# Performance work log

Hardware: AMD Instinct MI355X
Metric: run time of the kernel (lower is better)

The kernel has to match this reference:

```python
import jax, jax.numpy as jnp
import numpy as np

B, C, D, H, CS = 2, 1024, 512, 8, 64  # batch, bindings, d_binding, heads, chunk_size


def setup_inputs() -> dict:
    key = jax.random.key(0)
    ks = jax.random.split(key, 12)
    d = D // H
    def lin(k, out_f, in_f):
        return jax.random.normal(k, (out_f, in_f), jnp.float32) * (1.0 / np.sqrt(in_f))
    return {
        "x": jax.random.normal(ks[0], (B, C, D), jnp.float32),
        "Wq": lin(ks[1], D, D), "bq": jnp.zeros((D,), jnp.float32),
        "Wk": lin(ks[2], D, D), "bk": jnp.zeros((D,), jnp.float32),
        "Wv": lin(ks[3], D, D), "bv": jnp.zeros((D,), jnp.float32),
        "w1": lin(ks[4], d, 3 * d), "b1": jnp.zeros((d,), jnp.float32),
        "w2": lin(ks[5], 1, d), "b2": jnp.zeros((1,), jnp.float32),
        "Wo": lin(ks[6], D, D), "bo": jnp.zeros((D,), jnp.float32),
    }


def reference(x, Wq, bq, Wk, bk, Wv, bv, w1, b1, w2, b2, Wo, bo):
    Bx, Cx, Dx = x.shape
    d = Dx // H
    def heads(W, b):
        y = jnp.einsum('bcD,eD->bce', x, W) + b
        return y.reshape(Bx, Cx, H, d).transpose(0, 2, 1, 3)  # (B,H,C,d)
    q = heads(Wq, bq)
    k = heads(Wk, bk)
    v = heads(Wv, bv)
    # split first MLP layer weight into q / k / q*k blocks
    w1_q, w1_k, w1_qk = w1[:, :d], w1[:, d:2 * d], w1[:, 2 * d:]
    qp = jnp.einsum('bhcd,ed->bhce', q, w1_q)  # (B,H,C,d)
    kp = jnp.einsum('bhcd,ed->bhce', k, w1_k)  # (B,H,C,d)
    nc = Cx // CS
    q_ch = q.reshape(Bx, H, nc, CS, d).transpose(2, 0, 1, 3, 4)   # (nc,B,H,CS,d)
    qp_ch = qp.reshape(Bx, H, nc, CS, d).transpose(2, 0, 1, 3, 4)
    inv_sqrt_d = jnp.float32(1.0 / np.sqrt(d))

    def step(carry, xs):
        qc, qpc = xs  # (B,H,CS,d) each
        # hidden: (B,H,CS,C,d)
        res = qpc[:, :, :, None, :] + kp[:, :, None, :, :] + b1
        inter = qc[:, :, :, None, :] * k[:, :, None, :, :]
        hid = res + jnp.einsum('bhijd,ed->bhije', inter, w1_qk)
        h = jax.nn.gelu(hid, approximate=False)
        scores = (jnp.einsum('bhije,e->bhij', h, w2[0]) + b2[0]) * inv_sqrt_d
        attn = jax.nn.softmax(scores, axis=-1)  # (B,H,CS,C)
        out = jnp.einsum('bhij,bhjd->bhid', attn, v)  # (B,H,CS,d)
        return carry, out

    _, outs = jax.lax.scan(jax.checkpoint(step), None, (q_ch, qp_ch))  # (nc,B,H,CS,d)
    out = outs.transpose(1, 2, 0, 3, 4).reshape(Bx, H, Cx, d)
    out = out.transpose(0, 2, 1, 3).reshape(Bx, Cx, Dx)
    return jnp.einsum('bcD,eD->bce', out, Wo) + bo
```

## Files before the change

### kernel.cpp

```cpp
#include <hip/hip_runtime.h>
#include <cstdint>

typedef unsigned short u16;
typedef unsigned int u32;
typedef __attribute__((ext_vector_type(8))) short short8;
typedef __attribute__((ext_vector_type(4))) float floatx4;

__device__ __forceinline__ float b2f(u16 u) {
    union { unsigned int i; float f; } c; c.i = ((unsigned int)u) << 16; return c.f;
}
__device__ __forceinline__ u16 f2b(float f) {
    union { float f; unsigned int i; } c; c.f = f;
    unsigned int u = c.i;
    u = u + 0x7FFFu + ((u >> 16) & 1u);
    return (u16)(u >> 16);
}
__device__ __forceinline__ float rdlane(float v, int l) {
    union { float f; int i; } c; c.f = v;
    union { int i; float f; } o; o.i = __builtin_amdgcn_readlane(c.i, l);
    return o.f;
}
__device__ __forceinline__ float u2f(u32 u) { union { u32 u; float f; } c; c.u = u; return c.f; }

__global__ __launch_bounds__(256) void gemm_qkv(
    const float* __restrict__ x,
    const float* __restrict__ Wq, const float* __restrict__ Wk, const float* __restrict__ Wv,
    const float* __restrict__ bq, const float* __restrict__ bk, const float* __restrict__ bv,
    float* __restrict__ qout, u16* __restrict__ kout, float* __restrict__ vout)
{
    __shared__ u16 xs[64 * 72];
    __shared__ u16 wsl[64 * 72];
    int tid = threadIdx.x;
    int lane = tid & 63;
    int wv = tid >> 6;
    int lo = lane & 15, hi = lane >> 4;
    int which = blockIdx.y >> 3;
    int m0 = blockIdx.x * 64, n0 = (blockIdx.y & 7) * 64;
    const float* W    = which == 0 ? Wq : (which == 1 ? Wk : Wv);
    const float* bias = which == 0 ? bq : (which == 1 ? bk : bv);

    floatx4 acc[4];
#pragma unroll
    for (int mt = 0; mt < 4; ++mt) acc[mt] = (floatx4){0.f, 0.f, 0.f, 0.f};

    for (int k0 = 0; k0 < 512; k0 += 64) {
        __syncthreads();
#pragma unroll
        for (int i = 0; i < 2; ++i) {
            int v = tid + i * 256;
            int row = v >> 3, c8 = (v & 7) * 8;
            const float* ap = x + (m0 + row) * 512 + k0 + c8;
            const float* wp = W + (n0 + row) * 512 + k0 + c8;
            float4 a0 = *(const float4*)(ap);
            float4 a1 = *(const float4*)(ap + 4);
            float4 w0 = *(const float4*)(wp);
            float4 w1v = *(const float4*)(wp + 4);
            union { u16 u[8]; uint4 q; } ca, cw;
            ca.u[0] = f2b(a0.x); ca.u[1] = f2b(a0.y); ca.u[2] = f2b(a0.z); ca.u[3] = f2b(a0.w);
            ca.u[4] = f2b(a1.x); ca.u[5] = f2b(a1.y); ca.u[6] = f2b(a1.z); ca.u[7] = f2b(a1.w);
            cw.u[0] = f2b(w0.x); cw.u[1] = f2b(w0.y); cw.u[2] = f2b(w0.z); cw.u[3] = f2b(w0.w);
            cw.u[4] = f2b(w1v.x); cw.u[5] = f2b(w1v.y); cw.u[6] = f2b(w1v.z); cw.u[7] = f2b(w1v.w);
            *(uint4*)(xs + row * 72 + c8)  = ca.q;
            *(uint4*)(wsl + row * 72 + c8) = cw.q;
        }
        __syncthreads();
#pragma unroll
        for (int ks = 0; ks < 2; ++ks) {
            short8 bfr = *(const short8*)(wsl + (wv * 16 + lo) * 72 + ks * 32 + hi * 8);
#pragma unroll
            for (int mt = 0; mt < 4; ++mt) {
                short8 afr = *(const short8*)(xs + (mt * 16 + lo) * 72 + ks * 32 + hi * 8);
                acc[mt] = __builtin_amdgcn_mfma_f32_16x16x32_bf16(afr, bfr, acc[mt], 0, 0, 0);
            }
        }
    }

    int n = n0 + wv * 16 + lo;
    float bv2 = bias[n];
    int h = n >> 6, dd = n & 63;
#pragma unroll
    for (int mt = 0; mt < 4; ++mt) {
#pragma unroll
        for (int r = 0; r < 4; ++r) {
            int m = m0 + mt * 16 + hi * 4 + r;
            float y = acc[mt][r] + bv2;
            int b = m >> 10, c = m & 1023;
            int idx = (((b * 8 + h) * 1024) + c) * 64 + dd;
            if (which == 0)      qout[idx] = y;
            else if (which == 1) kout[idx] = f2b(y);
            else                 vout[idx] = y;
        }
    }
}

__global__ __launch_bounds__(256) void gemm_out(
    const float* __restrict__ A, const float* __restrict__ W, const float* __restrict__ bias,
    float* __restrict__ outf)
{
    __shared__ u16 xs[64 * 72];
    __shared__ u16 wsl[64 * 72];
    int tid = threadIdx.x;
    int lane = tid & 63;
    int wv = tid >> 6;
    int lo = lane & 15, hi = lane >> 4;
    int m0 = blockIdx.x * 64, n0 = blockIdx.y * 64;

    floatx4 acc[4];
#pragma unroll
    for (int mt = 0; mt < 4; ++mt) acc[mt] = (floatx4){0.f, 0.f, 0.f, 0.f};

    for (int k0 = 0; k0 < 512; k0 += 64) {
        __syncthreads();
#pragma unroll
        for (int i = 0; i < 2; ++i) {
            int v = tid + i * 256;
            int row = v >> 3, c8 = (v & 7) * 8;
            const float* ap = A + (m0 + row) * 512 + k0 + c8;
            const float* wp = W + (n0 + row) * 512 + k0 + c8;
            float4 a0 = *(const float4*)(ap);
            float4 a1 = *(const float4*)(ap + 4);
            float4 w0 = *(const float4*)(wp);
            float4 w1v = *(const float4*)(wp + 4);
            union { u16 u[8]; uint4 q; } ca, cw;
            ca.u[0] = f2b(a0.x); ca.u[1] = f2b(a0.y); ca.u[2] = f2b(a0.z); ca.u[3] = f2b(a0.w);
            ca.u[4] = f2b(a1.x); ca.u[5] = f2b(a1.y); ca.u[6] = f2b(a1.z); ca.u[7] = f2b(a1.w);
            cw.u[0] = f2b(w0.x); cw.u[1] = f2b(w0.y); cw.u[2] = f2b(w0.z); cw.u[3] = f2b(w0.w);
            cw.u[4] = f2b(w1v.x); cw.u[5] = f2b(w1v.y); cw.u[6] = f2b(w1v.z); cw.u[7] = f2b(w1v.w);
            *(uint4*)(xs + row * 72 + c8)  = ca.q;
            *(uint4*)(wsl + row * 72 + c8) = cw.q;
        }
        __syncthreads();
#pragma unroll
        for (int ks = 0; ks < 2; ++ks) {
            short8 bfr = *(const short8*)(wsl + (wv * 16 + lo) * 72 + ks * 32 + hi * 8);
#pragma unroll
            for (int mt = 0; mt < 4; ++mt) {
                short8 afr = *(const short8*)(xs + (mt * 16 + lo) * 72 + ks * 32 + hi * 8);
                acc[mt] = __builtin_amdgcn_mfma_f32_16x16x32_bf16(afr, bfr, acc[mt], 0, 0, 0);
            }
        }
    }

    int n = n0 + wv * 16 + lo;
    float bv = bias[n];
#pragma unroll
    for (int mt = 0; mt < 4; ++mt)
#pragma unroll
        for (int r = 0; r < 4; ++r) {
            int m = m0 + mt * 16 + hi * 4 + r;
            outf[m * 512 + n] = acc[mt][r] + bv;
        }
}

__global__ __launch_bounds__(256, 4) void attn13(
    const float* __restrict__ qf, const u16* __restrict__ kb, const float* __restrict__ vf,
    const float* __restrict__ w1, const float* __restrict__ b1, const float* __restrict__ w2,
    float* __restrict__ ao)
{
    __shared__ float q_l[4 * 64];
    int tid = threadIdx.x;
    int lane = tid & 63;
    int wv = tid >> 6;
    int lo = lane & 15, hi = lane >> 4;
    int bh = blockIdx.x >> 8;
    int qi = ((blockIdx.x & 255) << 2) | wv;

    const float NA = -2.45546696f;

    q_l[wv * 64 + lane] = qf[(bh * 1024 + qi) * 64 + lane];

    float qpacc = b1[lane];
#pragma unroll
    for (int d8 = 0; d8 < 64; d8 += 8) {
        float4 wa = *(const float4*)(w1 + lane * 192 + d8);
        float4 wb = *(const float4*)(w1 + lane * 192 + d8 + 4);
        const float* q8 = q_l + wv * 64 + d8;
        qpacc = __builtin_fmaf(q8[0], wa.x, qpacc);
        qpacc = __builtin_fmaf(q8[1], wa.y, qpacc);
        qpacc = __builtin_fmaf(q8[2], wa.z, qpacc);
        qpacc = __builtin_fmaf(q8[3], wa.w, qpacc);
        qpacc = __builtin_fmaf(q8[4], wb.x, qpacc);
        qpacc = __builtin_fmaf(q8[5], wb.y, qpacc);
        qpacc = __builtin_fmaf(q8[6], wb.z, qpacc);
        qpacc = __builtin_fmaf(q8[7], wb.w, qpacc);
    }
    qpacc *= NA;

    u32 wcp[4][2];
    float w2row = w2[lane] * -0.07344288f;
#pragma unroll
    for (int mt = 0; mt < 4; ++mt)
#pragma unroll
        for (int h2 = 0; h2 < 2; ++h2) {
            int e0 = mt * 16 + hi * 4 + h2 * 2;
            u32 lo16 = (u32)f2b(__shfl(w2row, e0));
            u32 hi16 = (u32)f2b(__shfl(w2row, e0 + 1));
            wcp[mt][h2] = (hi16 << 16) | lo16;
        }

    float qv2[2][8];
#pragma unroll
    for (int ks = 0; ks < 2; ++ks)
#pragma unroll
        for (int j = 0; j < 8; ++j)
            qv2[ks][j] = q_l[wv * 64 + ks * 32 + hi * 8 + j];

    short8 af[4][2];
#pragma unroll
    for (int mt = 0; mt < 4; ++mt) {
        const float* wr = w1 + (mt * 16 + lo) * 192;
#pragma unroll
        for (int ks = 0; ks < 2; ++ks) {
            int dd0 = ks * 32 + hi * 8;
            float4 a0 = *(const float4*)(wr + 128 + dd0);
            float4 a1 = *(const float4*)(wr + 128 + dd0 + 4);
            float4 k0 = *(const float4*)(wr + 64 + dd0);
            float4 k1 = *(const float4*)(wr + 64 + dd0 + 4);
            union { u16 u[8]; short8 s; } cv;
            cv.u[0] = f2b(NA * __builtin_fmaf(qv2[ks][0], a0.x, k0.x));
            cv.u[1] = f2b(NA * __builtin_fmaf(qv2[ks][1], a0.y, k0.y));
            cv.u[2] = f2b(NA * __builtin_fmaf(qv2[ks][2], a0.z, k0.z));
            cv.u[3] = f2b(NA * __builtin_fmaf(qv2[ks][3], a0.w, k0.w));
            cv.u[4] = f2b(NA * __builtin_fmaf(qv2[ks][4], a1.x, k1.x));
            cv.u[5] = f2b(NA * __builtin_fmaf(qv2[ks][5], a1.y, k1.y));
            cv.u[6] = f2b(NA * __builtin_fmaf(qv2[ks][6], a1.z, k1.z));
            cv.u[7] = f2b(NA * __builtin_fmaf(qv2[ks][7], a1.w, k1.w));
            af[mt][ks] = cv.s;
        }
    }

    floatx4 qpinit[4];
    {
        const floatx4 z = (floatx4){0.f, 0.f, 0.f, 0.f};
        union { u16 u[8]; short8 s; } bb;
#pragma unroll
        for (int i = 0; i < 8; ++i) bb.u[i] = 0;
        bb.u[0] = (hi == 0) ? (u16)0x3F80 : (u16)0;
#pragma unroll
        for (int mt = 0; mt < 4; ++mt) {
            float qpv = __shfl(qpacc, mt * 16 + lo);
            union { u16 u[8]; short8 s; } aa;
#pragma unroll
            for (int i = 0; i < 8; ++i) aa.u[i] = 0;
            aa.u[0] = (hi == 0) ? f2b(qpv) : (u16)0;
            qpinit[mt] = __builtin_amdgcn_mfma_f32_16x16x32_bf16(aa.s, bb.s, z, 0, 0, 0);
        }
    }

    float l_run = 0.f;
    float oa0 = 0.f, oa1 = 0.f, oa2 = 0.f, oa3 = 0.f;
    const u16*   kbase = kb + bh * 65536;
    const float* vbase = vf + bh * 65536;

    short8 bf[2][2];
#pragma unroll
    for (int t = 0; t < 2; ++t)
#pragma unroll
        for (int ks = 0; ks < 2; ++ks) {
            uint4 kv = *(const uint4*)(kbase + (t * 16 + lo) * 64 + ks * 32 + hi * 8);
            bf[t][ks] = *(short8*)&kv;
        }

    for (int j0 = 0; j0 < 1024; j0 += 32) {
        float s0a = 0.f, s0b = 0.f, s1a = 0.f, s1b = 0.f;

        floatx4 aP[2], aN[2];
        aP[0] = __builtin_amdgcn_mfma_f32_16x16x32_bf16(af[0][0], bf[0][0], qpinit[0], 0, 0, 0);
        aP[0] = __builtin_amdgcn_mfma_f32_16x16x32_bf16(af[0][1], bf[0][1], aP[0], 0, 0, 0);
        aP[1] = __builtin_amdgcn_mfma_f32_16x16x32_bf16(af[0][0], bf[1][0], qpinit[0], 0, 0, 0);
        aP[1] = __builtin_amdgcn_mfma_f32_16x16x32_bf16(af[0][1], bf[1][1], aP[1], 0, 0, 0);

#pragma unroll
        for (int mt = 0; mt < 4; ++mt) {
            if (mt < 3) {
                aN[0] = __builtin_amdgcn_mfma_f32_16x16x32_bf16(af[mt + 1][0], bf[0][0], qpinit[mt + 1], 0, 0, 0);
                aN[0] = __builtin_amdgcn_mfma_f32_16x16x32_bf16(af[mt + 1][1], bf[0][1], aN[0], 0, 0, 0);
                aN[1] = __builtin_amdgcn_mfma_f32_16x16x32_bf16(af[mt + 1][0], bf[1][0], qpinit[mt + 1], 0, 0, 0);
                aN[1] = __builtin_amdgcn_mfma_f32_16x16x32_bf16(af[mt + 1][1], bf[1][1], aN[1], 0, 0, 0);
            } else {
                int jn = (j0 + 32) & 1023;
#pragma unroll
                for (int t = 0; t < 2; ++t)
#pragma unroll
                    for (int ks = 0; ks < 2; ++ks) {
                        uint4 kv = *(const uint4*)(kbase + (jn + t * 16 + lo) * 64 + ks * 32 + hi * 8);
                        bf[t][ks] = *(short8*)&kv;
                    }
            }

#pragma unroll
            for (int h2 = 0; h2 < 2; ++h2) {
                u32 wp = wcp[mt][h2];
                float w0 = u2f(wp << 16);
                float w1v = u2f(wp & 0xFFFF0000u);
#pragma unroll
                for (int t = 0; t < 2; ++t) {
                    float x0 = aP[t][h2 * 2 + 0];
                    float x1 = aP[t][h2 * 2 + 1];
                    float a0 = 1.0f + __builtin_amdgcn_exp2f(x0);
                    float a1 = 1.0f + __builtin_amdgcn_exp2f(x1);
                    float rc = __builtin_amdgcn_rcpf(a0 * a1);
                    if (t == 0) {
                        s0a = __builtin_fmaf(x0 * w0,  rc * a1, s0a);
                        s0b = __builtin_fmaf(x1 * w1v, rc * a0, s0b);
                    } else {
                        s1a = __builtin_fmaf(x0 * w0,  rc * a1, s1a);
                        s1b = __builtin_fmaf(x1 * w1v, rc * a0, s1b);
                    }
                }
            }
            aP[0] = aN[0];
            aP[1] = aN[1];
        }

        float s0 = s0a + s0b, s1 = s1a + s1b;
        s0 += __shfl_xor(s0, 16); s0 += __shfl_xor(s0, 32);
        s1 += __shfl_xor(s1, 16); s1 += __shfl_xor(s1, 32);

        float p0 = __builtin_amdgcn_exp2f(s0 - 16.0f);
        float p1 = __builtin_amdgcn_exp2f(s1 - 16.0f);
        l_run += p0 + p1;

        const float* vrow = vbase + j0 * 64 + lane;
#pragma unroll
        for (int j = 0; j < 16; j += 4) {
            float pa0 = rdlane(p0, j + 0), pb0 = rdlane(p1, j + 0);
            float pa1 = rdlane(p0, j + 1), pb1 = rdlane(p1, j + 1);
            float pa2 = rdlane(p0, j + 2), pb2 = rdlane(p1, j + 2);
            float pa3 = rdlane(p0, j + 3), pb3 = rdlane(p1, j + 3);
            oa0 = __builtin_fmaf(pa0, vrow[(j + 0) * 64], oa0);
            oa1 = __builtin_fmaf(pa1, vrow[(j + 1) * 64], oa1);
            oa2 = __builtin_fmaf(pa2, vrow[(j + 2) * 64], oa2);
            oa3 = __builtin_fmaf(pa3, vrow[(j + 3) * 64], oa3);
            oa0 = __builtin_fmaf(pb0, vrow[(j + 16) * 64], oa0);
            oa1 = __builtin_fmaf(pb1, vrow[(j + 17) * 64], oa1);
            oa2 = __builtin_fmaf(pb2, vrow[(j + 18) * 64], oa2);
            oa3 = __builtin_fmaf(pb3, vrow[(j + 19) * 64], oa3);
        }
    }

    float l = l_run;
    l += __shfl_xor(l, 1); l += __shfl_xor(l, 2);
    l += __shfl_xor(l, 4); l += __shfl_xor(l, 8);
    float outv = (oa0 + oa1 + oa2 + oa3) * __builtin_amdgcn_rcpf(l);
    int b = bh >> 3, h = bh & 7;
    ao[(b * 1024 + qi) * 512 + h * 64 + lane] = outv;
}

extern "C" void kernel_launch(void* const* d_in, const int* in_sizes, int n_in,
                              void* d_out, int out_size, void* d_ws, size_t ws_size,
                              hipStream_t stream)
{
    (void)in_sizes; (void)n_in; (void)out_size; (void)ws_size;
    const float* x  = (const float*)d_in[0];
    const float* Wq = (const float*)d_in[1];
    const float* bq = (const float*)d_in[2];
    const float* Wk = (const float*)d_in[3];
    const float* bk = (const float*)d_in[4];
    const float* Wv = (const float*)d_in[5];
    const float* bv = (const float*)d_in[6];
    const float* w1 = (const float*)d_in[7];
    const float* b1 = (const float*)d_in[8];
    const float* w2 = (const float*)d_in[9];
    const float* Wo = (const float*)d_in[11];
    const float* bo = (const float*)d_in[12];

    char* ws = (char*)d_ws;
    float* q_ws = (float*)(ws);
    u16*   k_ws = (u16*)(ws + (4u << 20));
    float* v_ws = (float*)(ws + (6u << 20));
    float* a_ws = (float*)(ws + (10u << 20));

    dim3 blk(256);
    hipLaunchKernelGGL(gemm_qkv, dim3(32, 24), blk, 0, stream,
                       x, Wq, Wk, Wv, bq, bk, bv, q_ws, k_ws, v_ws);
    hipLaunchKernelGGL(attn13, dim3(4096), blk, 0, stream, q_ws, k_ws, v_ws, w1, b1, w2, a_ws);
    hipLaunchKernelGGL(gemm_out, dim3(32, 8), blk, 0, stream, a_ws, Wo, bo, (float*)d_out);
}
```

Before: 554.5 us.

## Compute P·V with MFMA using transposed split-bf16 V and shared-memory P exchange

The QKV GEMM now writes V transposed per head as hi/lo bf16 pairs through shared memory. The attention kernel no longer does the P·V product with scalar FMAs and readlane broadcasts. Each block writes bf16 probabilities for its 4 query rows into a double-buffered LDS tile, and two MFMAs per 32-key chunk (hi and lo V parts) accumulate the output. This moves the PV work onto matrix cores and cuts V load traffic. In exchange it adds a block-wide barrier per chunk, rounds P to bf16, and wastes most of each MFMA's M dimension, since only 4 query rows are used.

```diff
diff --git a/kernel.cpp b/kernel.cpp
--- a/kernel.cpp
+++ b/kernel.cpp
@@ -15,18 +15,14 @@
     u = u + 0x7FFFu + ((u >> 16) & 1u);
     return (u16)(u >> 16);
 }
-__device__ __forceinline__ float rdlane(float v, int l) {
-    union { float f; int i; } c; c.f = v;
-    union { int i; float f; } o; o.i = __builtin_amdgcn_readlane(c.i, l);
-    return o.f;
-}
 __device__ __forceinline__ float u2f(u32 u) { union { u32 u; float f; } c; c.u = u; return c.f; }
 
 __global__ __launch_bounds__(256) void gemm_qkv(
     const float* __restrict__ x,
     const float* __restrict__ Wq, const float* __restrict__ Wk, const float* __restrict__ Wv,
     const float* __restrict__ bq, const float* __restrict__ bk, const float* __restrict__ bv,
-    float* __restrict__ qout, u16* __restrict__ kout, float* __restrict__ vout)
+    float* __restrict__ qout, u16* __restrict__ kout,
+    u16* __restrict__ vthi, u16* __restrict__ vtlo)
 {
     __shared__ u16 xs[64 * 72];
     __shared__ u16 wsl[64 * 72];
@@ -77,19 +73,41 @@
 
     int n = n0 + wv * 16 + lo;
     float bv2 = bias[n];
-    int h = n >> 6, dd = n & 63;
-#pragma unroll
-    for (int mt = 0; mt < 4; ++mt) {
-#pragma unroll
-        for (int r = 0; r < 4; ++r) {
-            int m = m0 + mt * 16 + hi * 4 + r;
-            float y = acc[mt][r] + bv2;
-            int b = m >> 10, c = m & 1023;
-            int idx = (((b * 8 + h) * 1024) + c) * 64 + dd;
-            if (which == 0)      qout[idx] = y;
-            else if (which == 1) kout[idx] = f2b(y);
-            else                 vout[idx] = y;
-        }
+    if (which == 2) {
+        __syncthreads();
+        int nl = wv * 16 + lo;
+#pragma unroll
+        for (int mt = 0; mt < 4; ++mt)
+#pragma unroll
+            for (int r = 0; r < 4; ++r) {
+                int ml = mt * 16 + hi * 4 + r;
+                float y = acc[mt][r] + bv2;
+                u16 vh = f2b(y);
+                u16 vl = f2b(y - b2f(vh));
+                xs[nl * 72 + ml]  = vh;
+                wsl[nl * 72 + ml] = vl;
+            }
+        __syncthreads();
+        int row = tid >> 2, seg = (tid & 3) * 16;
+        int b = m0 >> 10, c0 = m0 & 1023, h2 = n0 >> 6;
+        size_t dst = ((size_t)((b * 8 + h2) * 64 + row)) * 1024 + c0 + seg;
+        *(uint4*)(vthi + dst)     = *(uint4*)(xs  + row * 72 + seg);
+        *(uint4*)(vthi + dst + 8) = *(uint4*)(xs  + row * 72 + seg + 8);
+        *(uint4*)(vtlo + dst)     = *(uint4*)(wsl + row * 72 + seg);
+        *(uint4*)(vtlo + dst + 8) = *(uint4*)(wsl + row * 72 + seg + 8);
+    } else {
+        int h = n >> 6, dd = n & 63;
+#pragma unroll
+        for (int mt = 0; mt < 4; ++mt)
+#pragma unroll
+            for (int r = 0; r < 4; ++r) {
+                int m = m0 + mt * 16 + hi * 4 + r;
+                float y = acc[mt][r] + bv2;
+                int b = m >> 10, c = m & 1023;
+                int idx = (((b * 8 + h) * 1024) + c) * 64 + dd;
+                if (which == 0) qout[idx] = y;
+                else            kout[idx] = f2b(y);
+            }
     }
 }
 
@@ -152,20 +170,26 @@
         }
 }
 
-__global__ __launch_bounds__(256, 4) void attn13(
-    const float* __restrict__ qf, const u16* __restrict__ kb, const float* __restrict__ vf,
+__global__ __launch_bounds__(256, 4) void attn14(
+    const float* __restrict__ qf, const u16* __restrict__ kb,
+    const u16* __restrict__ vthi, const u16* __restrict__ vtlo,
     const float* __restrict__ w1, const float* __restrict__ b1, const float* __restrict__ w2,
     float* __restrict__ ao)
 {
     __shared__ float q_l[4 * 64];
+    __shared__ __align__(16) u16 plds[2][512];
+    __shared__ float l_sh[4];
     int tid = threadIdx.x;
     int lane = tid & 63;
     int wv = tid >> 6;
     int lo = lane & 15, hi = lane >> 4;
     int bh = blockIdx.x >> 8;
-    int qi = ((blockIdx.x & 255) << 2) | wv;
+    int qbase = (blockIdx.x & 255) << 2;
+    int qi = qbase | wv;
 
     const float NA = -2.45546696f;
+
+    if (tid < 128) { uint4 z; z.x = z.y = z.z = z.w = 0u; ((uint4*)plds)[tid] = z; }
 
     q_l[wv * 64 + lane] = qf[(bh * 1024 + qi) * 64 + lane];
 
@@ -248,9 +272,10 @@
     }
 
     float l_run = 0.f;
-    float oa0 = 0.f, oa1 = 0.f, oa2 = 0.f, oa3 = 0.f;
-    const u16*   kbase = kb + bh * 65536;
-    const float* vbase = vf + bh * 65536;
+    floatx4 pvacc = (floatx4){0.f, 0.f, 0.f, 0.f};
+    const u16* kbase = kb + bh * 65536;
+    const u16* vhb = vthi + bh * 65536 + (wv * 16 + lo) * 1024 + hi * 8;
+    const u16* vlb = vtlo + bh * 65536 + (wv * 16 + lo) * 1024 + hi * 8;
 
     short8 bf[2][2];
 #pragma unroll
@@ -262,6 +287,9 @@
         }
 
     for (int j0 = 0; j0 < 1024; j0 += 32) {
+        uint4 vhq = *(const uint4*)(vhb + j0);
+        uint4 vlq = *(const uint4*)(vlb + j0);
+
         float s0a = 0.f, s0b = 0.f, s1a = 0.f, s1b = 0.f;
 
         floatx4 aP[2], aN[2];
@@ -319,32 +347,36 @@
 
         float p0 = __builtin_amdgcn_exp2f(s0 - 16.0f);
         float p1 = __builtin_amdgcn_exp2f(s1 - 16.0f);
-        l_run += p0 + p1;
-
-        const float* vrow = vbase + j0 * 64 + lane;
-#pragma unroll
-        for (int j = 0; j < 16; j += 4) {
-            float pa0 = rdlane(p0, j + 0), pb0 = rdlane(p1, j + 0);
-            float pa1 = rdlane(p0, j + 1), pb1 = rdlane(p1, j + 1);
-            float pa2 = rdlane(p0, j + 2), pb2 = rdlane(p1, j + 2);
-            float pa3 = rdlane(p0, j + 3), pb3 = rdlane(p1, j + 3);
-            oa0 = __builtin_fmaf(pa0, vrow[(j + 0) * 64], oa0);
-            oa1 = __builtin_fmaf(pa1, vrow[(j + 1) * 64], oa1);
-            oa2 = __builtin_fmaf(pa2, vrow[(j + 2) * 64], oa2);
-            oa3 = __builtin_fmaf(pa3, vrow[(j + 3) * 64], oa3);
-            oa0 = __builtin_fmaf(pb0, vrow[(j + 16) * 64], oa0);
-            oa1 = __builtin_fmaf(pb1, vrow[(j + 17) * 64], oa1);
-            oa2 = __builtin_fmaf(pb2, vrow[(j + 18) * 64], oa2);
-            oa3 = __builtin_fmaf(pb3, vrow[(j + 19) * 64], oa3);
-        }
+        u16 ph0 = f2b(p0);
+        u16 ph1 = f2b(p1);
+        l_run += b2f(ph0) + b2f(ph1);
+
+        u16* pw = (u16*)plds[(j0 >> 5) & 1];
+        if (lane < 16) {
+            pw[((lo >> 3) * 16 + wv) * 8 + (lo & 7)] = ph0;
+            pw[((2 + (lo >> 3)) * 16 + wv) * 8 + (lo & 7)] = ph1;
+        }
+        __syncthreads();
+
+        short8 pf = *(const short8*)(pw + lane * 8);
+        pvacc = __builtin_amdgcn_mfma_f32_16x16x32_bf16(pf, *(short8*)&vhq, pvacc, 0, 0, 0);
+        pvacc = __builtin_amdgcn_mfma_f32_16x16x32_bf16(pf, *(short8*)&vlq, pvacc, 0, 0, 0);
     }
 
     float l = l_run;
     l += __shfl_xor(l, 1); l += __shfl_xor(l, 2);
     l += __shfl_xor(l, 4); l += __shfl_xor(l, 8);
-    float outv = (oa0 + oa1 + oa2 + oa3) * __builtin_amdgcn_rcpf(l);
-    int b = bh >> 3, h = bh & 7;
-    ao[(b * 1024 + qi) * 512 + h * 64 + lane] = outv;
+    if (lane == 0) l_sh[wv] = l;
+    __syncthreads();
+
+    if (hi == 0) {
+        int b = bh >> 3, h = bh & 7;
+#pragma unroll
+        for (int q = 0; q < 4; ++q) {
+            float outv = pvacc[q] * __builtin_amdgcn_rcpf(l_sh[q]);
+            ao[((b * 1024 + qbase + q) * 512) + h * 64 + wv * 16 + lo] = outv;
+        }
+    }
 }
 
 extern "C" void kernel_launch(void* const* d_in, const int* in_sizes, int n_in,
@@ -368,12 +400,14 @@
     char* ws = (char*)d_ws;
     float* q_ws = (float*)(ws);
     u16*   k_ws = (u16*)(ws + (4u << 20));
-    float* v_ws = (float*)(ws + (6u << 20));
+    u16*   vthi = (u16*)(ws + (6u << 20));
+    u16*   vtlo = (u16*)(ws + (8u << 20));
     float* a_ws = (float*)(ws + (10u << 20));
 
     dim3 blk(256);
     hipLaunchKernelGGL(gemm_qkv, dim3(32, 24), blk, 0, stream,
-                       x, Wq, Wk, Wv, bq, bk, bv, q_ws, k_ws, v_ws);
-    hipLaunchKernelGGL(attn13, dim3(4096), blk, 0, stream, q_ws, k_ws, v_ws, w1, b1, w2, a_ws);
+                       x, Wq, Wk, Wv, bq, bk, bv, q_ws, k_ws, vthi, vtlo);
+    hipLaunchKernelGGL(attn14, dim3(4096), blk, 0, stream,
+                       q_ws, k_ws, vthi, vtlo, w1, b1, w2, a_ws);
     hipLaunchKernelGGL(gemm_out, dim3(32, 8), blk, 0, stream, a_ws, Wo, bo, (float*)d_out);
 }
```

Result: no change. 555.6 us (+0.2%).
